# Optimization experiments

Measured on AMD Instinct MI355X. Metric: run time of the kernel, lower is better.

The kernel has to match this reference:

```python
import jax, jax.numpy as jnp
import numpy as np

C = 128

def setup_inputs() -> dict:
    key = jax.random.key(0)
    ks = jax.random.split(key, 8)
    x = jax.random.normal(ks[0], (8, C, 64, 64), dtype=jnp.float32)
    y = jax.random.normal(ks[1], (8, C, 32, 32), dtype=jnp.float32)
    s = 1.0 / np.sqrt(C)
    Wq = jax.random.normal(ks[2], (C, C), dtype=jnp.float32) * s
    bq = jnp.zeros((C,), dtype=jnp.float32)
    Wk = jax.random.normal(ks[3], (C, C), dtype=jnp.float32) * s
    bk = jnp.zeros((C,), dtype=jnp.float32)
    Wv = jax.random.normal(ks[4], (C, C), dtype=jnp.float32) * s
    bv = jnp.zeros((C,), dtype=jnp.float32)
    return {"x": x, "y": y, "Wq": Wq, "bq": bq, "Wk": Wk, "bk": bk, "Wv": Wv, "bv": bv}


def reference(x, y, Wq, bq, Wk, bk, Wv, bv):
    B, C_, H, W = x.shape
    # flatten spatial -> tokens: (B, N, C)
    x_flat = x.reshape(B, C_, H * W).transpose(0, 2, 1)
    y_flat = y.reshape(B, C_, -1).transpose(0, 2, 1)
    # torch Linear: out = in @ W.T + b
    Q = jnp.einsum('bnc,dc->bnd', x_flat, Wq) + bq
    K = jnp.einsum('bmc,dc->bmd', y_flat, Wk) + bk
    V = jnp.einsum('bmc,dc->bmd', y_flat, Wv) + bv
    scale = 1.0 / jnp.sqrt(jnp.asarray(C_, dtype=x.dtype))
    scores = jnp.einsum('bnd,bmd->bnm', Q, K) * scale  # (B, HW, H'W')
    attn = jax.nn.softmax(scores, axis=-1)
    z = jnp.einsum('bnm,bmd->bnd', attn, V)
    z = z.transpose(0, 2, 1).reshape(B, C_, H, W)
    return x + z
```

## Files before the change

kernel.cpp:

```cpp
#include <hip/hip_runtime.h>

#define BB 8
#define NN 4096
#define MMK 1024
#define SCLL2E 0.12751743f
#define SM2 2.88539008f

typedef __bf16 v8bf __attribute__((ext_vector_type(8)));
typedef float v4f __attribute__((ext_vector_type(4)));
typedef float v16f __attribute__((ext_vector_type(16)));
#define MFMA16 __builtin_amdgcn_mfma_f32_16x16x32_bf16
#define MFMA32F8 __builtin_amdgcn_mfma_f32_32x32x16_fp8_fp8

static __device__ __forceinline__ unsigned pk4(float a, float b, float c, float d) {
    int u = __builtin_amdgcn_cvt_pk_fp8_f32(a, b, 0, false);
    u = __builtin_amdgcn_cvt_pk_fp8_f32(c, d, u, true);
    return (unsigned)u;
}
static __device__ __forceinline__ long long mk64(unsigned lo, unsigned hi) {
    return (long long)(((unsigned long long)hi << 32) | lo);
}
static __device__ __forceinline__ long long lo64(uint4 u) { return mk64(u.x, u.y); }
static __device__ __forceinline__ long long hi64(uint4 u) { return mk64(u.z, u.w); }

static __device__ __forceinline__ float exp2_fast(float x) {
#if __has_builtin(__builtin_amdgcn_exp2f)
    return __builtin_amdgcn_exp2f(x);
#else
    float r;
    asm("v_exp_f32 %0, %1" : "=v"(r) : "v"(x));
    return r;
#endif
}

#define COMPUTE_S(DST, KB)                                                  \
    do {                                                                    \
        v16f a_;                                                            \
        _Pragma("unroll")                                                   \
        for (int r_ = 0; r_ < 16; ++r_) a_[r_] = 0.f;                       \
        __builtin_amdgcn_s_setprio(1);                                      \
        a_ = MFMA32F8(lo64(KB[0]), lo64(qv[0]), a_, 0, 0, 0);               \
        a_ = MFMA32F8(hi64(KB[0]), hi64(qv[0]), a_, 0, 0, 0);               \
        a_ = MFMA32F8(lo64(KB[1]), lo64(qv[1]), a_, 0, 0, 0);               \
        a_ = MFMA32F8(hi64(KB[1]), hi64(qv[1]), a_, 0, 0, 0);               \
        a_ = MFMA32F8(lo64(KB[2]), lo64(qv[2]), a_, 0, 0, 0);               \
        a_ = MFMA32F8(hi64(KB[2]), hi64(qv[2]), a_, 0, 0, 0);               \
        a_ = MFMA32F8(lo64(KB[3]), lo64(qv[3]), a_, 0, 0, 0);               \
        a_ = MFMA32F8(hi64(KB[3]), hi64(qv[3]), a_, 0, 0, 0);               \
        __builtin_amdgcn_s_setprio(0);                                      \
        DST = a_;                                                           \
    } while (0)

#define XTS 68
#define WTS 136
__global__ __launch_bounds__(256, 1) void proj(
    const float* __restrict__ x, const float* __restrict__ y,
    const float* __restrict__ Wq, const float* __restrict__ bq,
    const float* __restrict__ Wk, const float* __restrict__ bk,
    const float* __restrict__ Wv, const float* __restrict__ bv,
    unsigned char* __restrict__ Qfr, unsigned char* __restrict__ Kfr,
    unsigned char* __restrict__ Vfr)
{
    __shared__ __align__(16) __bf16 xt[128 * XTS];
    __shared__ __align__(16) __bf16 wt[128 * WTS];
    __shared__ float bsh[128];

    const int tid = threadIdx.x;
    const int wave = tid >> 6, lane = tid & 63, l15 = lane & 15, quad = lane >> 4;
    const int bid = blockIdx.x;

    int job, b, t0, stride;
    const float *in, *W, *bias;
    if (bid < 512)      { job = 0; b = bid >> 6;         t0 = (bid & 63) * 64;         in = x; stride = NN;  W = Wq; bias = bq; }
    else if (bid < 640) { job = 1; b = (bid - 512) >> 4; t0 = ((bid - 512) & 15) * 64; in = y; stride = MMK; W = Wk; bias = bk; }
    else                { job = 2; b = (bid - 640) >> 4; t0 = ((bid - 640) & 15) * 64; in = y; stride = MMK; W = Wv; bias = bv; }

    #pragma unroll
    for (int i = 0; i < 8; ++i) {
        const int s = i * 256 + tid;
        const int c = s >> 4, c4 = s & 15;
        float4 v = *(const float4*)(in + (size_t)(b * 128 + c) * stride + t0 + c4 * 4);
        union { __bf16 h[4]; uint2 u; } o;
        o.h[0] = (__bf16)v.x; o.h[1] = (__bf16)v.y; o.h[2] = (__bf16)v.z; o.h[3] = (__bf16)v.w;
        *(uint2*)(xt + c * XTS + c4 * 4) = o.u;
    }
    #pragma unroll
    for (int i = 0; i < 16; ++i) {
        const int f = i * 1024 + tid * 4;
        const int d = f >> 7, c = f & 127;
        float4 v = *(const float4*)(W + f);
        union { __bf16 h[4]; uint2 u; } o;
        o.h[0] = (__bf16)v.x; o.h[1] = (__bf16)v.y; o.h[2] = (__bf16)v.z; o.h[3] = (__bf16)v.w;
        *(uint2*)(wt + d * WTS + c) = o.u;
    }
    if (tid < 128) bsh[tid] = bias[tid];
    __syncthreads();

    v8bf xf[4];
    {
        const int tok = wave * 16 + l15;
        #pragma unroll
        for (int cg = 0; cg < 4; ++cg) {
            union { __bf16 h[8]; v8bf v; } u;
            #pragma unroll
            for (int jj = 0; jj < 8; ++jj)
                u.h[jj] = xt[(cg * 32 + quad * 8 + jj) * XTS + tok];
            xf[cg] = u.v;
        }
    }

    for (int dg = 0; dg < 8; ++dg) {
        const __bf16* wrow = wt + (dg * 16 + l15) * WTS + quad * 8;
        v8bf wf[4];
        #pragma unroll
        for (int cg = 0; cg < 4; ++cg)
            wf[cg] = *(const v8bf*)(wrow + cg * 32);

        float4 b4 = *(const float4*)(bsh + dg * 16 + quad * 4);
        v4f acc;
        acc[0] = b4.x; acc[1] = b4.y; acc[2] = b4.z; acc[3] = b4.w;
        #pragma unroll
        for (int cg = 0; cg < 4; ++cg)
            acc = MFMA16(wf[cg], xf[cg], acc, 0, 0, 0);

        const int tok = t0 + wave * 16 + l15;
        const int d0 = dg * 16 + quad * 4;
        const unsigned u32 = pk4(acc[0], acc[1], acc[2], acc[3]);

        if (job <= 1) {
            unsigned char* Out = (job == 0) ? Qfr : Kfr;
            const int tiles = (job == 0) ? 128 : 32;
            const size_t off = ((size_t)(b * tiles + (tok >> 5)) * 4 + (d0 >> 5)) * 1024
                             + ((d0 >> 3) & 1) * 512 + (tok & 31) * 16
                             + ((d0 >> 4) & 1) * 8 + (d0 & 7);
            *(unsigned*)(Out + off) = u32;
        } else {
            #pragma unroll
            for (int r = 0; r < 4; ++r) {
                const int ch = d0 + r, key = tok;
                const size_t off = ((size_t)(b * 32 + (key >> 5)) * 4 + (ch >> 5)) * 1024
                                 + ((key >> 3) & 1) * 512 + (ch & 31) * 16
                                 + ((key >> 4) & 1) * 8 + (key & 7);
                Vfr[off] = (unsigned char)(u32 >> (8 * r));
            }
        }
    }
}

__global__ __launch_bounds__(256, 2) void attn(
    const float* __restrict__ x, const unsigned char* __restrict__ Qfr,
    const unsigned char* __restrict__ Kfr, const unsigned char* __restrict__ Vfr,
    float* __restrict__ out)
{
    __shared__ float Oacc[2][128 * 32];
    __shared__ float Lacc[2][2][32];

    const int tid = threadIdx.x;
    const int wave = tid >> 6, lane = tid & 63, r31 = lane & 31, h = lane >> 5;
    const int qs = wave >> 1;
    const int kh = wave & 1;
    const int b = blockIdx.x >> 6;
    const int qt = (blockIdx.x & 63) * 2 + qs;

    const uint4* Qc = (const uint4*)Qfr + (size_t)(b * 128 + qt) * 4 * 64;
    const uint4* Kc = (const uint4*)Kfr + (size_t)(b * 32 + kh * 16) * 4 * 64;
    const uint4* Vc = (const uint4*)Vfr + (size_t)(b * 32 + kh * 16) * 4 * 64;

    uint4 qv[4];
    #pragma unroll
    for (int s2 = 0; s2 < 4; ++s2) qv[s2] = Qc[s2 * 64 + lane];

    v16f o[4];
    #pragma unroll
    for (int cg = 0; cg < 4; ++cg)
        #pragma unroll
        for (int r = 0; r < 16; ++r) o[cg][r] = 0.f;
    float l0 = 0.f, l1 = 0.f, l2 = 0.f, l3 = 0.f;

    uint4 kb[2][4], vb[2][4];
    #pragma unroll
    for (int s2 = 0; s2 < 4; ++s2) kb[0][s2] = Kc[s2 * 64 + lane];
    #pragma unroll
    for (int s2 = 0; s2 < 4; ++s2) vb[0][s2] = Vc[s2 * 64 + lane];
    #pragma unroll
    for (int s2 = 0; s2 < 4; ++s2) kb[1][s2] = Kc[(4 + s2) * 64 + lane];
    #pragma unroll
    for (int s2 = 0; s2 < 4; ++s2) vb[1][s2] = Vc[(4 + s2) * 64 + lane];

    v16f S;
    COMPUTE_S(S, kb[0]);

    #pragma unroll
    for (int j = 0; j < 16; ++j) {
        const int cur = j & 1, nxt = (j + 1) & 1;

        if ((j & 3) == 0) __builtin_amdgcn_s_barrier();

        if (j < 14) {
            #pragma unroll
            for (int s2 = 0; s2 < 4; ++s2)
                kb[cur][s2] = Kc[((j + 2) * 4 + s2) * 64 + lane];
        }

        float p[16];
        #pragma unroll
        for (int r = 0; r < 16; ++r) p[r] = exp2_fast(fmaf(S[r], SCLL2E, -SM2));
        #pragma unroll
        for (int r = 0; r < 4; ++r) {
            l0 += p[r]; l1 += p[4 + r]; l2 += p[8 + r]; l3 += p[12 + r];
        }

        const unsigned qa = pk4(p[0], p[1], p[2], p[3]);
        const unsigned qb = pk4(p[4], p[5], p[6], p[7]);
        const unsigned qc = pk4(p[8], p[9], p[10], p[11]);
        const unsigned qd = pk4(p[12], p[13], p[14], p[15]);
        long long pf0, pf1;
#if __has_builtin(__builtin_amdgcn_permlane32_swap)
        {
            auto r0 = __builtin_amdgcn_permlane32_swap((int)qa, (int)qb, false, false);
            auto r1 = __builtin_amdgcn_permlane32_swap((int)qc, (int)qd, false, false);
            pf0 = mk64((unsigned)r0[0], (unsigned)r0[1]);
            pf1 = mk64((unsigned)r1[0], (unsigned)r1[1]);
        }
#else
        {
            unsigned e0 = h ? qa : qb; e0 = __shfl_xor(e0, 32);
            unsigned e1 = h ? qc : qd; e1 = __shfl_xor(e1, 32);
            pf0 = mk64(h ? e0 : qa, h ? qb : e0);
            pf1 = mk64(h ? e1 : qc, h ? qd : e1);
        }
#endif

        v16f Sn = S;
        if (j < 15) COMPUTE_S(Sn, kb[nxt]);

        __builtin_amdgcn_s_setprio(1);
        #pragma unroll
        for (int cg = 0; cg < 4; ++cg) {
            o[cg] = MFMA32F8(lo64(vb[cur][cg]), pf0, o[cg], 0, 0, 0);
            o[cg] = MFMA32F8(hi64(vb[cur][cg]), pf1, o[cg], 0, 0, 0);
        }
        __builtin_amdgcn_s_setprio(0);

        if (j < 14) {
            #pragma unroll
            for (int s2 = 0; s2 < 4; ++s2)
                vb[cur][s2] = Vc[((j + 2) * 4 + s2) * 64 + lane];
        }

        S = Sn;
    }

    float l = (l0 + l1) + (l2 + l3);
    l += __shfl_xor(l, 32);
    if (h == 0) Lacc[qs][kh][r31] = l;
    if (kh == 0) {
        #pragma unroll
        for (int cg = 0; cg < 4; ++cg)
            #pragma unroll
            for (int r = 0; r < 16; ++r) {
                const int ch = cg * 32 + (r & 3) + 8 * (r >> 2) + 4 * h;
                Oacc[qs][ch * 32 + r31] = o[cg][r];
            }
    }
    __syncthreads();
    if (kh == 1) {
        #pragma unroll
        for (int cg = 0; cg < 4; ++cg)
            #pragma unroll
            for (int r = 0; r < 16; ++r) {
                const int ch = cg * 32 + (r & 3) + 8 * (r >> 2) + 4 * h;
                Oacc[qs][ch * 32 + r31] += o[cg][r];
            }
    }
    __syncthreads();

    const float linv = 1.0f / (Lacc[qs][0][r31] + Lacc[qs][1][r31]);

    #pragma unroll
    for (int i = 0; i < 32; ++i) {
        const int ch = (kh * 2 + h) + i * 4;
        const float val = Oacc[qs][ch * 32 + r31] * linv;
        const size_t gi = (size_t)(b * 128 + ch) * NN + qt * 32 + r31;
        out[gi] = x[gi] + val;
    }
}

extern "C" void kernel_launch(void* const* d_in, const int* in_sizes, int n_in,
                              void* d_out, int out_size, void* d_ws, size_t ws_size,
                              hipStream_t stream) {
    const float* x  = (const float*)d_in[0];
    const float* y  = (const float*)d_in[1];
    const float* Wq = (const float*)d_in[2];
    const float* bq = (const float*)d_in[3];
    const float* Wk = (const float*)d_in[4];
    const float* bk = (const float*)d_in[5];
    const float* Wv = (const float*)d_in[6];
    const float* bv = (const float*)d_in[7];
    float* out = (float*)d_out;

    unsigned char* Qfr = (unsigned char*)d_ws;
    unsigned char* Kfr = Qfr + (size_t)BB * NN * 128;
    unsigned char* Vfr = Kfr + (size_t)BB * MMK * 128;

    proj<<<768, 256, 0, stream>>>(x, y, Wq, bq, Wk, bk, Wv, bv, Qfr, Kfr, Vfr);
    attn<<<BB * (NN / 64), 256, 0, stream>>>(x, Qfr, Kfr, Vfr, out);
}
```

Baseline: 107.8 us.

## Fuse Q projection into attention kernel, keep Q tile in shared memory

The Q projection moves out of the proj kernel and into the attention kernel. Each attention block now loads its 64-token x tile and Wq, computes Q with bf16 MFMA, and packs it as fp8 into shared memory, so Q no longer makes a round trip through global memory and the proj grid shrinks to K/V only. The cost is that every attention block reloads and converts the full Wq, and its prologue gets longer. The staging buffers share a union with the reduction buffers, which adds a sync, and the larger shared-memory footprint may limit occupancy.

```diff
diff --git a/kernel.cpp b/kernel.cpp
--- a/kernel.cpp
+++ b/kernel.cpp
@@ -53,13 +53,12 @@
 
 #define XTS 68
 #define WTS 136
+
 __global__ __launch_bounds__(256, 1) void proj(
-    const float* __restrict__ x, const float* __restrict__ y,
-    const float* __restrict__ Wq, const float* __restrict__ bq,
+    const float* __restrict__ y,
     const float* __restrict__ Wk, const float* __restrict__ bk,
     const float* __restrict__ Wv, const float* __restrict__ bv,
-    unsigned char* __restrict__ Qfr, unsigned char* __restrict__ Kfr,
-    unsigned char* __restrict__ Vfr)
+    unsigned char* __restrict__ Kfr, unsigned char* __restrict__ Vfr)
 {
     __shared__ __align__(16) __bf16 xt[128 * XTS];
     __shared__ __align__(16) __bf16 wt[128 * WTS];
@@ -69,17 +68,16 @@
     const int wave = tid >> 6, lane = tid & 63, l15 = lane & 15, quad = lane >> 4;
     const int bid = blockIdx.x;
 
-    int job, b, t0, stride;
-    const float *in, *W, *bias;
-    if (bid < 512)      { job = 0; b = bid >> 6;         t0 = (bid & 63) * 64;         in = x; stride = NN;  W = Wq; bias = bq; }
-    else if (bid < 640) { job = 1; b = (bid - 512) >> 4; t0 = ((bid - 512) & 15) * 64; in = y; stride = MMK; W = Wk; bias = bk; }
-    else                { job = 2; b = (bid - 640) >> 4; t0 = ((bid - 640) & 15) * 64; in = y; stride = MMK; W = Wv; bias = bv; }
+    int job, b, t0;
+    const float *W, *bias;
+    if (bid < 128) { job = 1; b = bid >> 4;         t0 = (bid & 15) * 64;         W = Wk; bias = bk; }
+    else           { job = 2; b = (bid - 128) >> 4; t0 = ((bid - 128) & 15) * 64; W = Wv; bias = bv; }
 
     #pragma unroll
     for (int i = 0; i < 8; ++i) {
         const int s = i * 256 + tid;
         const int c = s >> 4, c4 = s & 15;
-        float4 v = *(const float4*)(in + (size_t)(b * 128 + c) * stride + t0 + c4 * 4);
+        float4 v = *(const float4*)(y + (size_t)(b * 128 + c) * MMK + t0 + c4 * 4);
         union { __bf16 h[4]; uint2 u; } o;
         o.h[0] = (__bf16)v.x; o.h[1] = (__bf16)v.y; o.h[2] = (__bf16)v.z; o.h[3] = (__bf16)v.w;
         *(uint2*)(xt + c * XTS + c4 * 4) = o.u;
@@ -127,13 +125,11 @@
         const int d0 = dg * 16 + quad * 4;
         const unsigned u32 = pk4(acc[0], acc[1], acc[2], acc[3]);
 
-        if (job <= 1) {
-            unsigned char* Out = (job == 0) ? Qfr : Kfr;
-            const int tiles = (job == 0) ? 128 : 32;
-            const size_t off = ((size_t)(b * tiles + (tok >> 5)) * 4 + (d0 >> 5)) * 1024
+        if (job == 1) {
+            const size_t off = ((size_t)(b * 32 + (tok >> 5)) * 4 + (d0 >> 5)) * 1024
                              + ((d0 >> 3) & 1) * 512 + (tok & 31) * 16
                              + ((d0 >> 4) & 1) * 8 + (d0 & 7);
-            *(unsigned*)(Out + off) = u32;
+            *(unsigned*)(Kfr + off) = u32;
         } else {
             #pragma unroll
             for (int r = 0; r < 4; ++r) {
@@ -148,27 +144,90 @@
 }
 
 __global__ __launch_bounds__(256, 2) void attn(
-    const float* __restrict__ x, const unsigned char* __restrict__ Qfr,
+    const float* __restrict__ x, const float* __restrict__ Wq,
+    const float* __restrict__ bq,
     const unsigned char* __restrict__ Kfr, const unsigned char* __restrict__ Vfr,
     float* __restrict__ out)
 {
-    __shared__ float Oacc[2][128 * 32];
-    __shared__ float Lacc[2][2][32];
+    __shared__ union SMem {
+        struct { __align__(16) __bf16 xt[128 * XTS];
+                 __align__(16) __bf16 wt[128 * WTS];
+                 float bsh[128]; } p0;
+        struct { float Oacc[2][128 * 32];
+                 float Lacc[2][2][32]; } p1;
+    } sm;
+    __shared__ __align__(16) uint4 Qsh[2][256];
 
     const int tid = threadIdx.x;
     const int wave = tid >> 6, lane = tid & 63, r31 = lane & 31, h = lane >> 5;
+    const int l15 = lane & 15, quad = lane >> 4;
     const int qs = wave >> 1;
     const int kh = wave & 1;
     const int b = blockIdx.x >> 6;
+    const int t0 = (blockIdx.x & 63) * 64;
     const int qt = (blockIdx.x & 63) * 2 + qs;
 
-    const uint4* Qc = (const uint4*)Qfr + (size_t)(b * 128 + qt) * 4 * 64;
+    #pragma unroll
+    for (int i = 0; i < 8; ++i) {
+        const int s = i * 256 + tid;
+        const int c = s >> 4, c4 = s & 15;
+        float4 v = *(const float4*)(x + (size_t)(b * 128 + c) * NN + t0 + c4 * 4);
+        union { __bf16 h[4]; uint2 u; } o;
+        o.h[0] = (__bf16)v.x; o.h[1] = (__bf16)v.y; o.h[2] = (__bf16)v.z; o.h[3] = (__bf16)v.w;
+        *(uint2*)(sm.p0.xt + c * XTS + c4 * 4) = o.u;
+    }
+    #pragma unroll
+    for (int i = 0; i < 16; ++i) {
+        const int f = i * 1024 + tid * 4;
+        const int d = f >> 7, c = f & 127;
+        float4 v = *(const float4*)(Wq + f);
+        union { __bf16 h[4]; uint2 u; } o;
+        o.h[0] = (__bf16)v.x; o.h[1] = (__bf16)v.y; o.h[2] = (__bf16)v.z; o.h[3] = (__bf16)v.w;
+        *(uint2*)(sm.p0.wt + d * WTS + c) = o.u;
+    }
+    if (tid < 128) sm.p0.bsh[tid] = bq[tid];
+    __syncthreads();
+
+    {
+        const int tokl = wave * 16 + l15;
+        v8bf xf[4];
+        #pragma unroll
+        for (int cg = 0; cg < 4; ++cg) {
+            union { __bf16 h[8]; v8bf v; } u;
+            #pragma unroll
+            for (int jj = 0; jj < 8; ++jj)
+                u.h[jj] = sm.p0.xt[(cg * 32 + quad * 8 + jj) * XTS + tokl];
+            xf[cg] = u.v;
+        }
+        #pragma unroll
+        for (int dg = 0; dg < 8; ++dg) {
+            const __bf16* wrow = sm.p0.wt + (dg * 16 + l15) * WTS + quad * 8;
+            v8bf wf[4];
+            #pragma unroll
+            for (int cg = 0; cg < 4; ++cg)
+                wf[cg] = *(const v8bf*)(wrow + cg * 32);
+            float4 b4 = *(const float4*)(sm.p0.bsh + dg * 16 + quad * 4);
+            v4f acc;
+            acc[0] = b4.x; acc[1] = b4.y; acc[2] = b4.z; acc[3] = b4.w;
+            #pragma unroll
+            for (int cg = 0; cg < 4; ++cg)
+                acc = MFMA16(wf[cg], xf[cg], acc, 0, 0, 0);
+            const int d0 = dg * 16 + quad * 4;
+            const unsigned u32 = pk4(acc[0], acc[1], acc[2], acc[3]);
+            const size_t off = (size_t)(tokl >> 5) * 4096 + (d0 >> 5) * 1024
+                             + ((d0 >> 3) & 1) * 512 + (tokl & 31) * 16
+                             + ((d0 >> 4) & 1) * 8 + (d0 & 7);
+            *(unsigned*)((char*)Qsh + off) = u32;
+        }
+    }
+    __syncthreads();
+
     const uint4* Kc = (const uint4*)Kfr + (size_t)(b * 32 + kh * 16) * 4 * 64;
     const uint4* Vc = (const uint4*)Vfr + (size_t)(b * 32 + kh * 16) * 4 * 64;
 
     uint4 qv[4];
     #pragma unroll
-    for (int s2 = 0; s2 < 4; ++s2) qv[s2] = Qc[s2 * 64 + lane];
+    for (int s2 = 0; s2 < 4; ++s2) qv[s2] = Qsh[qs][s2 * 64 + lane];
 
     v16f o[4];
     #pragma unroll
@@ -253,14 +312,15 @@
 
     float l = (l0 + l1) + (l2 + l3);
     l += __shfl_xor(l, 32);
-    if (h == 0) Lacc[qs][kh][r31] = l;
+    __syncthreads();
+    if (h == 0) sm.p1.Lacc[qs][kh][r31] = l;
     if (kh == 0) {
         #pragma unroll
         for (int cg = 0; cg < 4; ++cg)
             #pragma unroll
             for (int r = 0; r < 16; ++r) {
                 const int ch = cg * 32 + (r & 3) + 8 * (r >> 2) + 4 * h;
-                Oacc[qs][ch * 32 + r31] = o[cg][r];
+                sm.p1.Oacc[qs][ch * 32 + r31] = o[cg][r];
             }
     }
     __syncthreads();
@@ -270,17 +330,17 @@
             #pragma unroll
             for (int r = 0; r < 16; ++r) {
                 const int ch = cg * 32 + (r & 3) + 8 * (r >> 2) + 4 * h;
-                Oacc[qs][ch * 32 + r31] += o[cg][r];
+                sm.p1.Oacc[qs][ch * 32 + r31] += o[cg][r];
             }
     }
     __syncthreads();
 
-    const float linv = 1.0f / (Lacc[qs][0][r31] + Lacc[qs][1][r31]);
+    const float linv = 1.0f / (sm.p1.Lacc[qs][0][r31] + sm.p1.Lacc[qs][1][r31]);
 
     #pragma unroll
     for (int i = 0; i < 32; ++i) {
         const int ch = (kh * 2 + h) + i * 4;
-        const float val = Oacc[qs][ch * 32 + r31] * linv;
+        const float val = sm.p1.Oacc[qs][ch * 32 + r31] * linv;
         const size_t gi = (size_t)(b * 128 + ch) * NN + qt * 32 + r31;
         out[gi] = x[gi] + val;
     }
@@ -299,10 +359,9 @@
     const float* bv = (const float*)d_in[7];
     float* out = (float*)d_out;
 
-    unsigned char* Qfr = (unsigned char*)d_ws;
-    unsigned char* Kfr = Qfr + (size_t)BB * NN * 128;
+    unsigned char* Kfr = (unsigned char*)d_ws;
     unsigned char* Vfr = Kfr + (size_t)BB * MMK * 128;
 
-    proj<<<768, 256, 0, stream>>>(x, y, Wq, bq, Wk, bk, Wv, bv, Qfr, Kfr, Vfr);
-    attn<<<BB * (NN / 64), 256, 0, stream>>>(x, Qfr, Kfr, Vfr, out);
-}
+    proj<<<256, 256, 0, stream>>>(y, Wk, bk, Wv, bv, Kfr, Vfr);
+    attn<<<BB * (NN / 64), 256, 0, stream>>>(x, Wq, bq, Kfr, Vfr, out);
+}
```

Measured after the change: 107.0 us. Within noise of the previous version (-0.7%).
